# Kernel optimization log

Measured on AMD Instinct MI355X. Metric: run time of the kernel, lower is better.

The kernel has to match this reference:

```python
import jax, jax.numpy as jnp
import numpy as np

N = 50000      # nodes
E = 800000     # edges (avg degree 16)
H = 4          # attention heads
F_IN = 256     # input feature dim
D = 64         # per-head hidden/out dim (hidden*H = 256 chains into next layer)
NEG_SLOPE = 0.2  # DGL GATConv default leaky_relu slope


def setup_inputs() -> dict:
    key = jax.random.key(0)
    ks = jax.random.split(key, 12)
    inp = {
        "features": jax.random.normal(ks[0], (N, F_IN), jnp.float32),
        "src": jax.random.randint(ks[1], (E,), 0, N, jnp.int32),
        "dst": jax.random.randint(ks[2], (E,), 0, N, jnp.int32),
    }
    dims = [(F_IN, D), (H * D, D), (H * D, D)]
    for i, (fin, dout) in enumerate(dims):
        sc = 1.0 / np.sqrt(fin)
        inp[f"W{i+1}"] = jax.random.normal(ks[3 + 3 * i], (fin, H * dout), jnp.float32) * sc
        inp[f"al{i+1}"] = jax.random.normal(ks[4 + 3 * i], (H, dout), jnp.float32) * 0.1
        inp[f"ar{i+1}"] = jax.random.normal(ks[5 + 3 * i], (H, dout), jnp.float32) * 0.1
        inp[f"b{i+1}"] = jnp.zeros((H * dout,), jnp.float32)
    return inp


def gat_layer(h, src, dst, W, al, ar, b, act):
    n = h.shape[0]
    feat = (h @ W).reshape(n, H, -1)                     # [N, H, D]
    el = jnp.sum(feat * al, axis=-1)                     # [N, H]
    er = jnp.sum(feat * ar, axis=-1)                     # [N, H]
    e = jax.nn.leaky_relu(el[src] + er[dst], NEG_SLOPE)  # [E, H]
    # segment (per-dst) softmax over incoming edges
    m = jax.ops.segment_max(e, dst, num_segments=n)      # [N, H]
    ex = jnp.exp(e - m[dst])
    s = jax.ops.segment_sum(ex, dst, num_segments=n)
    alpha = ex / jnp.maximum(s[dst], 1e-9)               # [E, H]
    # weighted scatter-aggregate of source features
    out = jax.ops.segment_sum(feat[src] * alpha[..., None], dst, num_segments=n)  # [N, H, D]
    out = out + b.reshape(1, H, -1)
    if act:
        out = jax.nn.elu(out)
    return out.reshape(n, -1)                            # flatten(1): concat heads


def reference(features, src, dst, W1, al1, ar1, b1, W2, al2, ar2, b2, W3, al3, ar3, b3):
    h = gat_layer(features, src, dst, W1, al1, ar1, b1, act=True)
    h = gat_layer(h, src, dst, W2, al2, ar2, b2, act=True)
    h = gat_layer(h, src, dst, W3, al3, ar3, b3, act=False)
    return h  # [N, H*D] = [50000, 256]
```

## Files before the change

### kernel.cpp

```cpp
#include <hip/hip_runtime.h>
#include <hip/hip_bf16.h>
#include <cstdint>


#define FEAT 256
#define NHEAD 4

typedef short short8 __attribute__((ext_vector_type(8)));
typedef float f32x4 __attribute__((ext_vector_type(4)));

__device__ __forceinline__ ushort f2bf(float v) {
    uint u = __float_as_uint(v);
    uint r = (u + 0x7fffu + ((u >> 16) & 1u)) >> 16;
    return (ushort)r;
}
__device__ __forceinline__ float bf2f(ushort h) {
    return __uint_as_float(((uint)h) << 16);
}

__global__ void hist_kernel(const int* __restrict__ dst, int* __restrict__ deg, int E) {
    int e = blockIdx.x * 256 + threadIdx.x;
    if (e < E) atomicAdd(&deg[dst[e]], 1);
}

__global__ void scan_block(const int* __restrict__ deg, int* __restrict__ offs,
                           int* __restrict__ bsums, int n) {
    __shared__ int s[256];
    int i = blockIdx.x * 256 + threadIdx.x;
    int v = (i < n) ? deg[i] : 0;
    s[threadIdx.x] = v; __syncthreads();
    #pragma unroll
    for (int off = 1; off < 256; off <<= 1) {
        int t = (threadIdx.x >= off) ? s[threadIdx.x - off] : 0;
        __syncthreads();
        s[threadIdx.x] += t;
        __syncthreads();
    }
    if (i < n) offs[i] = s[threadIdx.x] - v;
    if (threadIdx.x == 255) bsums[blockIdx.x] = s[255];
}

__global__ void scan_sums(int* __restrict__ bsums, int nb) {
    __shared__ int s[256];
    int v = (threadIdx.x < nb) ? bsums[threadIdx.x] : 0;
    s[threadIdx.x] = v; __syncthreads();
    #pragma unroll
    for (int off = 1; off < 256; off <<= 1) {
        int t = (threadIdx.x >= off) ? s[threadIdx.x - off] : 0;
        __syncthreads();
        s[threadIdx.x] += t;
        __syncthreads();
    }
    if (threadIdx.x < nb) bsums[threadIdx.x] = s[threadIdx.x] - v;
}

__global__ void scan_add(int* __restrict__ offs, int* __restrict__ cursor,
                         const int* __restrict__ bsums, int n, int total) {
    int i = blockIdx.x * 256 + threadIdx.x;
    if (i < n) {
        int o = offs[i] + bsums[i >> 8];
        offs[i] = o;
        cursor[i] = o;
    }
    if (i == 0) offs[n] = total;
}

__global__ void scatter_kernel(const int* __restrict__ src, const int* __restrict__ dst,
                               int* __restrict__ cursor, int* __restrict__ csr_src, int E) {
    int e = blockIdx.x * 256 + threadIdx.x;
    if (e < E) {
        int d = dst[e];
        int pos = atomicAdd(&cursor[d], 1);
        csr_src[pos] = src[e];
    }
}

__global__ void wprep3_kernel(const float* __restrict__ W0, const float* __restrict__ W1,
                              const float* __restrict__ W2,
                              ushort* __restrict__ Wh0, ushort* __restrict__ Wl0,
                              ushort* __restrict__ Wh1, ushort* __restrict__ Wl1,
                              ushort* __restrict__ Wh2, ushort* __restrict__ Wl2) {
    const float* W = (blockIdx.y == 0) ? W0 : (blockIdx.y == 1) ? W1 : W2;
    ushort* Wh = (blockIdx.y == 0) ? Wh0 : (blockIdx.y == 1) ? Wh1 : Wh2;
    ushort* Wl = (blockIdx.y == 0) ? Wl0 : (blockIdx.y == 1) ? Wl1 : Wl2;
    int n = blockIdx.x;
    int k = threadIdx.x;
    float v = W[(size_t)k * FEAT + n];
    ushort h = f2bf(v);
    float r = v - bf2f(h);
    Wh[(size_t)n * FEAT + k] = h;
    Wl[(size_t)n * FEAT + k] = f2bf(r);
}

__global__ void fsplit_kernel(const float* __restrict__ A, ushort* __restrict__ Ah,
                              ushort* __restrict__ Al, int total8) {
    int i = blockIdx.x * 256 + threadIdx.x;
    if (i >= total8) return;
    const float4* p = (const float4*)(A + (size_t)i * 8);
    float4 a = p[0], b = p[1];
    float v[8] = {a.x, a.y, a.z, a.w, b.x, b.y, b.z, b.w};
    ushort hi[8], lo[8];
    #pragma unroll
    for (int t = 0; t < 8; ++t) {
        hi[t] = f2bf(v[t]);
        lo[t] = f2bf(v[t] - bf2f(hi[t]));
    }
    *(short8*)(Ah + (size_t)i * 8) = *(short8*)hi;
    *(short8*)(Al + (size_t)i * 8) = *(short8*)lo;
}

#define GBM 128
#define GBK 32
#define LDK 40
#define NKIT (FEAT / GBK)

__global__ __launch_bounds__(256) void gemm_fused(const ushort* __restrict__ Ahg,
                                                  const ushort* __restrict__ Alg,
                                                  const ushort* __restrict__ Whg,
                                                  const ushort* __restrict__ Wlg,
                                                  const float* __restrict__ alv,
                                                  const float* __restrict__ arv,
                                                  ushort* __restrict__ featB,
                                                  float* __restrict__ el,
                                                  float* __restrict__ er, int M) {
    __shared__ ushort Ah[2][GBM][LDK];
    __shared__ ushort Al[2][GBM][LDK];

    const int tid  = threadIdx.x;
    const int lane = tid & 63;
    const int wid  = tid >> 6;
    const int row0 = blockIdx.x * GBM;

    const int arow = tid >> 1;
    const int achk = (tid & 1) * 16;
    const bool aok = (row0 + arow) < M;
    const ushort* ApH = Ahg + (size_t)(row0 + arow) * FEAT + achk;
    const ushort* ApL = Alg + (size_t)(row0 + arow) * FEAT + achk;

    const int fr = lane & 15;
    const int fk = (lane >> 4) * 8;
    const int q  = lane >> 4;

    f32x4 acc[8][4];
    #pragma unroll
    for (int i = 0; i < 8; ++i)
        #pragma unroll
        for (int j = 0; j < 4; ++j) {
            f32x4 z = {0.f, 0.f, 0.f, 0.f};
            acc[i][j] = z;
        }

    const short8 z8 = {0, 0, 0, 0, 0, 0, 0, 0};

    {
        short8 h0 = aok ? *(const short8*)(ApH)     : z8;
        short8 h1 = aok ? *(const short8*)(ApH + 8) : z8;
        short8 l0 = aok ? *(const short8*)(ApL)     : z8;
        short8 l1 = aok ? *(const short8*)(ApL + 8) : z8;
        *(short8*)&Ah[0][arow][achk]     = h0;
        *(short8*)&Ah[0][arow][achk + 8] = h1;
        *(short8*)&Al[0][arow][achk]     = l0;
        *(short8*)&Al[0][arow][achk + 8] = l1;
    }

    #pragma unroll
    for (int t = 0; t < NKIT; ++t) {
        const int cur = t & 1;
        const int k0 = t * GBK;
        short8 h0 = z8, h1 = z8, l0 = z8, l1 = z8;
        if (t + 1 < NKIT && aok) {
            h0 = *(const short8*)(ApH + k0 + GBK);
            h1 = *(const short8*)(ApH + k0 + GBK + 8);
            l0 = *(const short8*)(ApL + k0 + GBK);
            l1 = *(const short8*)(ApL + k0 + GBK + 8);
        }
        short8 bfh[4], bfl[4];
        #pragma unroll
        for (int nt = 0; nt < 4; ++nt) {
            size_t boff = (size_t)(wid * 64 + nt * 16 + fr) * FEAT + k0 + fk;
            bfh[nt] = *(const short8*)(Whg + boff);
            bfl[nt] = *(const short8*)(Wlg + boff);
        }

        __syncthreads();

        #pragma unroll
        for (int mt = 0; mt < 8; ++mt) {
            short8 afh = *(const short8*)&Ah[cur][mt * 16 + fr][fk];
            short8 afl = *(const short8*)&Al[cur][mt * 16 + fr][fk];
            #pragma unroll
            for (int nt = 0; nt < 4; ++nt) {
                acc[mt][nt] = __builtin_amdgcn_mfma_f32_16x16x32_bf16(
                    afh, bfh[nt], acc[mt][nt], 0, 0, 0);
                acc[mt][nt] = __builtin_amdgcn_mfma_f32_16x16x32_bf16(
                    afh, bfl[nt], acc[mt][nt], 0, 0, 0);
                acc[mt][nt] = __builtin_amdgcn_mfma_f32_16x16x32_bf16(
                    afl, bfh[nt], acc[mt][nt], 0, 0, 0);
            }
        }
        if (t + 1 < NKIT) {
            *(short8*)&Ah[cur ^ 1][arow][achk]     = h0;
            *(short8*)&Ah[cur ^ 1][arow][achk + 8] = h1;
            *(short8*)&Al[cur ^ 1][arow][achk]     = l0;
            *(short8*)&Al[cur ^ 1][arow][achk + 8] = l1;
        }
    }

    float al4[4], ar4[4];
    #pragma unroll
    for (int nt = 0; nt < 4; ++nt) {
        al4[nt] = alv[wid * 64 + nt * 16 + fr];
        ar4[nt] = arv[wid * 64 + nt * 16 + fr];
    }
    #pragma unroll
    for (int mt = 0; mt < 8; ++mt) {
        #pragma unroll
        for (int r = 0; r < 4; ++r) {
            int row = row0 + mt * 16 + q * 4 + r;
            bool ok = row < M;
            float pl = 0.f, pr = 0.f;
            #pragma unroll
            for (int nt = 0; nt < 4; ++nt) {
                float v = acc[mt][nt][r];
                if (ok) featB[(size_t)row * FEAT + wid * 64 + nt * 16 + fr] = f2bf(v);
                pl = fmaf(v, al4[nt], pl);
                pr = fmaf(v, ar4[nt], pr);
            }
            #pragma unroll
            for (int o = 1; o < 16; o <<= 1) {
                pl += __shfl_xor(pl, o, 64);
                pr += __shfl_xor(pr, o, 64);
            }
            if (ok && fr == 0) {
                el[(size_t)row * NHEAD + wid] = pl;
                er[(size_t)row * NHEAD + wid] = pr;
            }
        }
    }
}

__global__ __launch_bounds__(256) void agg_kernel5(const ushort* __restrict__ featB,
                                                   const float* __restrict__ el,
                                                   const float* __restrict__ er,
                                                   const int* __restrict__ offs,
                                                   const int* __restrict__ csr_src,
                                                   const float* __restrict__ bias,
                                                   float* __restrict__ outF,
                                                   ushort* __restrict__ outH,
                                                   ushort* __restrict__ outL,
                                                   int act, int n) {
    int node = blockIdx.x * 4 + (threadIdx.x >> 6);
    if (node >= n) return;
    int lane = threadIdx.x & 63;
    int h   = lane >> 4;
    int j16 = lane & 15;
    int l31 = lane & 31;
    int par = lane >> 5;
    int fb  = l31 * 8;
    int hh  = l31 >> 3;
    int start = offs[node];
    int deg = offs[node + 1] - start;
    float erh = er[node * NHEAD + h];

    float m = -1e30f, ssum = 0.f;
    float a0 = 0.f, a1 = 0.f, a2 = 0.f, a3 = 0.f;
    float a4 = 0.f, a5 = 0.f, a6 = 0.f, a7 = 0.f;
    int sidx = (j16 < deg) ? csr_src[start + j16] : 0;

    for (int p0 = 0; p0 < deg; p0 += 16) {
        int pn = p0 + 16 + j16;
        int sidx_nx = (pn < deg) ? csr_src[start + pn] : 0;
        float e = -1e30f;
        if (p0 + j16 < deg) {
            float t = el[sidx * NHEAD + h] + erh;
            e = (t > 0.f) ? t : 0.2f * t;
        }
        float cm = e;
        #pragma unroll
        for (int o = 1; o < 16; o <<= 1) cm = fmaxf(cm, __shfl_xor(cm, o, 64));
        float newm = fmaxf(m, cm);
        float sc = __expf(m - newm);
        m = newm;
        ssum *= sc;
        float w = __expf(e - m);
        ssum += w;
        float scA = __shfl(sc, hh * 16, 64);
        a0 *= scA; a1 *= scA; a2 *= scA; a3 *= scA;
        a4 *= scA; a5 *= scA; a6 *= scA; a7 *= scA;
        int cnt = min(16, deg - p0);
        int iters = (cnt + 1) >> 1;
        for (int i = 0; i < iters; ++i) {
            int j0 = 2 * i + par;
            int sj = __shfl(sidx, j0, 16);
            float wj = __shfl(w, hh * 16 + j0, 64);
            short8 v = *(const short8*)(featB + (size_t)sj * FEAT + fb);
            a0 = fmaf(wj, bf2f((ushort)v[0]), a0);
            a1 = fmaf(wj, bf2f((ushort)v[1]), a1);
            a2 = fmaf(wj, bf2f((ushort)v[2]), a2);
            a3 = fmaf(wj, bf2f((ushort)v[3]), a3);
            a4 = fmaf(wj, bf2f((ushort)v[4]), a4);
            a5 = fmaf(wj, bf2f((ushort)v[5]), a5);
            a6 = fmaf(wj, bf2f((ushort)v[6]), a6);
            a7 = fmaf(wj, bf2f((ushort)v[7]), a7);
        }
        sidx = sidx_nx;
    }
    a0 += __shfl_xor(a0, 32, 64);
    a1 += __shfl_xor(a1, 32, 64);
    a2 += __shfl_xor(a2, 32, 64);
    a3 += __shfl_xor(a3, 32, 64);
    a4 += __shfl_xor(a4, 32, 64);
    a5 += __shfl_xor(a5, 32, 64);
    a6 += __shfl_xor(a6, 32, 64);
    a7 += __shfl_xor(a7, 32, 64);

    float st = ssum;
    #pragma unroll
    for (int o = 1; o < 16; o <<= 1) st += __shfl_xor(st, o, 64);
    float stA = __shfl(st, hh * 16, 64);
    if (par == 0) {
        float inv = 1.f / fmaxf(stA, 1e-9f);
        float4 b0 = *(const float4*)(bias + fb);
        float4 b1 = *(const float4*)(bias + fb + 4);
        float o0 = fmaf(a0, inv, b0.x);
        float o1 = fmaf(a1, inv, b0.y);
        float o2 = fmaf(a2, inv, b0.z);
        float o3 = fmaf(a3, inv, b0.w);
        float o4 = fmaf(a4, inv, b1.x);
        float o5 = fmaf(a5, inv, b1.y);
        float o6 = fmaf(a6, inv, b1.z);
        float o7 = fmaf(a7, inv, b1.w);
        if (act) {
            o0 = (o0 > 0.f) ? o0 : expm1f(o0);
            o1 = (o1 > 0.f) ? o1 : expm1f(o1);
            o2 = (o2 > 0.f) ? o2 : expm1f(o2);
            o3 = (o3 > 0.f) ? o3 : expm1f(o3);
            o4 = (o4 > 0.f) ? o4 : expm1f(o4);
            o5 = (o5 > 0.f) ? o5 : expm1f(o5);
            o6 = (o6 > 0.f) ? o6 : expm1f(o6);
            o7 = (o7 > 0.f) ? o7 : expm1f(o7);
        }
        if (outF) {
            *((float4*)(outF + (size_t)node * FEAT + fb))     = make_float4(o0, o1, o2, o3);
            *((float4*)(outF + (size_t)node * FEAT + fb + 4)) = make_float4(o4, o5, o6, o7);
        } else {
            ushort hi[8], lo[8];
            float ov[8] = {o0, o1, o2, o3, o4, o5, o6, o7};
            #pragma unroll
            for (int k = 0; k < 8; ++k) {
                hi[k] = f2bf(ov[k]);
                lo[k] = f2bf(ov[k] - bf2f(hi[k]));
            }
            *(short8*)(outH + (size_t)node * FEAT + fb) = *(short8*)hi;
            *(short8*)(outL + (size_t)node * FEAT + fb) = *(short8*)lo;
        }
    }
}

extern "C" void kernel_launch(void* const* d_in, const int* in_sizes, int n_in,
                              void* d_out, int out_size, void* d_ws, size_t ws_size,
                              hipStream_t stream) {
    const float* features = (const float*)d_in[0];
    const int*   src      = (const int*)d_in[1];
    const int*   dst      = (const int*)d_in[2];
    const int N = in_sizes[0] / FEAT;
    const int E = in_sizes[1];

    char* ws = (char*)d_ws;
    size_t off = 0;
    auto carve = [&](size_t bytes) -> void* {
        void* p = ws + off;
        off = (off + bytes + 255) & ~(size_t)255;
        return p;
    };
    int*    deg     = (int*)carve((size_t)N * 4);
    int*    offs    = (int*)carve((size_t)(N + 1) * 4);
    int*    cursor  = (int*)carve((size_t)N * 4);
    int*    bsums   = (int*)carve(4096);
    int*    csr_src = (int*)carve((size_t)E * 4);
    float*  el      = (float*)carve((size_t)N * NHEAD * 4);
    float*  er      = (float*)carve((size_t)N * NHEAD * 4);
    ushort* featB   = (ushort*)carve((size_t)N * FEAT * 2);
    ushort* inAh    = (ushort*)carve((size_t)N * FEAT * 2);
    ushort* inAl    = (ushort*)carve((size_t)N * FEAT * 2);
    ushort* Wh[3], *Wl[3];
    for (int i = 0; i < 3; ++i) {
        Wh[i] = (ushort*)carve((size_t)FEAT * FEAT * 2);
        Wl[i] = (ushort*)carve((size_t)FEAT * FEAT * 2);
    }

    const int nbE = (E + 255) / 256;
    const int nbN = (N + 255) / 256;

    hipMemsetAsync(deg, 0, (size_t)N * 4, stream);
    hist_kernel<<<nbE, 256, 0, stream>>>(dst, deg, E);
    scan_block<<<nbN, 256, 0, stream>>>(deg, offs, bsums, N);
    scan_sums<<<1, 256, 0, stream>>>(bsums, nbN);
    scan_add<<<nbN, 256, 0, stream>>>(offs, cursor, bsums, N, E);
    scatter_kernel<<<nbE, 256, 0, stream>>>(src, dst, cursor, csr_src, E);
    dim3 wgrid(FEAT, 3);
    wprep3_kernel<<<wgrid, FEAT, 0, stream>>>((const float*)d_in[3], (const float*)d_in[7],
                                              (const float*)d_in[11],
                                              Wh[0], Wl[0], Wh[1], Wl[1], Wh[2], Wl[2]);
    const int total8 = N * FEAT / 8;
    fsplit_kernel<<<(total8 + 255) / 256, 256, 0, stream>>>(features, inAh, inAl, total8);

    const int gemmBlocks = (N + GBM - 1) / GBM;
    const int nodeBlocks = (N + 3) / 4;

    gemm_fused<<<gemmBlocks, 256, 0, stream>>>(inAh, inAl, Wh[0], Wl[0],
                                               (const float*)d_in[4], (const float*)d_in[5],
                                               featB, el, er, N);
    agg_kernel5<<<nodeBlocks, 256, 0, stream>>>(featB, el, er, offs, csr_src,
                                                (const float*)d_in[6],
                                                (float*)nullptr, inAh, inAl, 1, N);
    gemm_fused<<<gemmBlocks, 256, 0, stream>>>(inAh, inAl, Wh[1], Wl[1],
                                               (const float*)d_in[8], (const float*)d_in[9],
                                               featB, el, er, N);
    agg_kernel5<<<nodeBlocks, 256, 0, stream>>>(featB, el, er, offs, csr_src,
                                                (const float*)d_in[10],
                                                (float*)nullptr, inAh, inAl, 1, N);
    gemm_fused<<<gemmBlocks, 256, 0, stream>>>(inAh, inAl, Wh[2], Wl[2],
                                               (const float*)d_in[12], (const float*)d_in[13],
                                               featB, el, er, N);
    agg_kernel5<<<nodeBlocks, 256, 0, stream>>>(featB, el, er, offs, csr_src,
                                                (const float*)d_in[14],
                                                (float*)d_out, (ushort*)nullptr, (ushort*)nullptr, 0, N);
}
```

Measured before the change: 474.0 us.

## Fuse fp32 hi/lo bf16 split into first-layer GEMM and halve GEMM row tile

```diff
diff --git a/kernel.cpp b/kernel.cpp
--- a/kernel.cpp
+++ b/kernel.cpp
@@ -92,24 +92,7 @@
     Wl[(size_t)n * FEAT + k] = f2bf(r);
 }
 
-__global__ void fsplit_kernel(const float* __restrict__ A, ushort* __restrict__ Ah,
-                              ushort* __restrict__ Al, int total8) {
-    int i = blockIdx.x * 256 + threadIdx.x;
-    if (i >= total8) return;
-    const float4* p = (const float4*)(A + (size_t)i * 8);
-    float4 a = p[0], b = p[1];
-    float v[8] = {a.x, a.y, a.z, a.w, b.x, b.y, b.z, b.w};
-    ushort hi[8], lo[8];
-    #pragma unroll
-    for (int t = 0; t < 8; ++t) {
-        hi[t] = f2bf(v[t]);
-        lo[t] = f2bf(v[t] - bf2f(hi[t]));
-    }
-    *(short8*)(Ah + (size_t)i * 8) = *(short8*)hi;
-    *(short8*)(Al + (size_t)i * 8) = *(short8*)lo;
-}
-
-#define GBM 128
+#define GBM 64
 #define GBK 32
 #define LDK 40
 #define NKIT (FEAT / GBK)
@@ -131,8 +114,8 @@
     const int wid  = tid >> 6;
     const int row0 = blockIdx.x * GBM;
 
-    const int arow = tid >> 1;
-    const int achk = (tid & 1) * 16;
+    const int arow = tid >> 2;
+    const int achk = (tid & 3) * 8;
     const bool aok = (row0 + arow) < M;
     const ushort* ApH = Ahg + (size_t)(row0 + arow) * FEAT + achk;
     const ushort* ApL = Alg + (size_t)(row0 + arow) * FEAT + achk;
@@ -141,9 +124,9 @@
     const int fk = (lane >> 4) * 8;
     const int q  = lane >> 4;
 
-    f32x4 acc[8][4];
-    #pragma unroll
-    for (int i = 0; i < 8; ++i)
+    f32x4 acc[4][4];
+    #pragma unroll
+    for (int i = 0; i < 4; ++i)
         #pragma unroll
         for (int j = 0; j < 4; ++j) {
             f32x4 z = {0.f, 0.f, 0.f, 0.f};
@@ -153,26 +136,20 @@
     const short8 z8 = {0, 0, 0, 0, 0, 0, 0, 0};
 
     {
-        short8 h0 = aok ? *(const short8*)(ApH)     : z8;
-        short8 h1 = aok ? *(const short8*)(ApH + 8) : z8;
-        short8 l0 = aok ? *(const short8*)(ApL)     : z8;
-        short8 l1 = aok ? *(const short8*)(ApL + 8) : z8;
-        *(short8*)&Ah[0][arow][achk]     = h0;
-        *(short8*)&Ah[0][arow][achk + 8] = h1;
-        *(short8*)&Al[0][arow][achk]     = l0;
-        *(short8*)&Al[0][arow][achk + 8] = l1;
+        short8 a_h = aok ? *(const short8*)(ApH) : z8;
+        short8 a_l = aok ? *(const short8*)(ApL) : z8;
+        *(short8*)&Ah[0][arow][achk] = a_h;
+        *(short8*)&Al[0][arow][achk] = a_l;
     }
 
     #pragma unroll
     for (int t = 0; t < NKIT; ++t) {
         const int cur = t & 1;
         const int k0 = t * GBK;
-        short8 h0 = z8, h1 = z8, l0 = z8, l1 = z8;
+        short8 a_h = z8, a_l = z8;
         if (t + 1 < NKIT && aok) {
-            h0 = *(const short8*)(ApH + k0 + GBK);
-            h1 = *(const short8*)(ApH + k0 + GBK + 8);
-            l0 = *(const short8*)(ApL + k0 + GBK);
-            l1 = *(const short8*)(ApL + k0 + GBK + 8);
+            a_h = *(const short8*)(ApH + k0 + GBK);
+            a_l = *(const short8*)(ApL + k0 + GBK);
         }
         short8 bfh[4], bfl[4];
         #pragma unroll
@@ -185,7 +162,7 @@
         __syncthreads();
 
         #pragma unroll
-        for (int mt = 0; mt < 8; ++mt) {
+        for (int mt = 0; mt < 4; ++mt) {
             short8 afh = *(const short8*)&Ah[cur][mt * 16 + fr][fk];
             short8 afl = *(const short8*)&Al[cur][mt * 16 + fr][fk];
             #pragma unroll
@@ -199,10 +176,8 @@
             }
         }
         if (t + 1 < NKIT) {
-            *(short8*)&Ah[cur ^ 1][arow][achk]     = h0;
-            *(short8*)&Ah[cur ^ 1][arow][achk + 8] = h1;
-            *(short8*)&Al[cur ^ 1][arow][achk]     = l0;
-            *(short8*)&Al[cur ^ 1][arow][achk + 8] = l1;
+            *(short8*)&Ah[cur ^ 1][arow][achk] = a_h;
+            *(short8*)&Al[cur ^ 1][arow][achk] = a_l;
         }
     }
 
@@ -213,7 +188,130 @@
         ar4[nt] = arv[wid * 64 + nt * 16 + fr];
     }
     #pragma unroll
-    for (int mt = 0; mt < 8; ++mt) {
+    for (int mt = 0; mt < 4; ++mt) {
+        #pragma unroll
+        for (int r = 0; r < 4; ++r) {
+            int row = row0 + mt * 16 + q * 4 + r;
+            bool ok = row < M;
+            float pl = 0.f, pr = 0.f;
+            #pragma unroll
+            for (int nt = 0; nt < 4; ++nt) {
+                float v = acc[mt][nt][r];
+                if (ok) featB[(size_t)row * FEAT + wid * 64 + nt * 16 + fr] = f2bf(v);
+                pl = fmaf(v, al4[nt], pl);
+                pr = fmaf(v, ar4[nt], pr);
+            }
+            #pragma unroll
+            for (int o = 1; o < 16; o <<= 1) {
+                pl += __shfl_xor(pl, o, 64);
+                pr += __shfl_xor(pr, o, 64);
+            }
+            if (ok && fr == 0) {
+                el[(size_t)row * NHEAD + wid] = pl;
+                er[(size_t)row * NHEAD + wid] = pr;
+            }
+        }
+    }
+}
+
+__global__ __launch_bounds__(256) void gemm_fused_f32a(const float* __restrict__ Af,
+                                                       const ushort* __restrict__ Whg,
+                                                       const ushort* __restrict__ Wlg,
+                                                       const float* __restrict__ alv,
+                                                       const float* __restrict__ arv,
+                                                       ushort* __restrict__ featB,
+                                                       float* __restrict__ el,
+                                                       float* __restrict__ er, int M) {
+    __shared__ ushort Ah[2][GBM][LDK];
+    __shared__ ushort Al[2][GBM][LDK];
+
+    const int tid  = threadIdx.x;
+    const int lane = tid & 63;
+    const int wid  = tid >> 6;
+    const int row0 = blockIdx.x * GBM;
+
+    const int arow = tid >> 2;
+    const int achk = (tid & 3) * 8;
+    const bool aok = (row0 + arow) < M;
+    const float* Ap = Af + (size_t)(row0 + arow) * FEAT + achk;
+
+    const int fr = lane & 15;
+    const int fk = (lane >> 4) * 8;
+    const int q  = lane >> 4;
+
+    f32x4 acc[4][4];
+    #pragma unroll
+    for (int i = 0; i < 4; ++i)
+        #pragma unroll
+        for (int j = 0; j < 4; ++j) {
+            f32x4 z = {0.f, 0.f, 0.f, 0.f};
+            acc[i][j] = z;
+        }
+
+    const float4 z4 = make_float4(0.f, 0.f, 0.f, 0.f);
+
+    auto split_store = [&](int buf, float4 f0, float4 f1) {
+        float v[8] = {f0.x, f0.y, f0.z, f0.w, f1.x, f1.y, f1.z, f1.w};
+        ushort hi[8], lo[8];
+        #pragma unroll
+        for (int k = 0; k < 8; ++k) {
+            hi[k] = f2bf(v[k]);
+            lo[k] = f2bf(v[k] - bf2f(hi[k]));
+        }
+        *(short8*)&Ah[buf][arow][achk] = *(short8*)hi;
+        *(short8*)&Al[buf][arow][achk] = *(short8*)lo;
+    };
+
+    {
+        float4 f0 = aok ? *(const float4*)(Ap)     : z4;
+        float4 f1 = aok ? *(const float4*)(Ap + 4) : z4;
+        split_store(0, f0, f1);
+    }
+
+    #pragma unroll
+    for (int t = 0; t < NKIT; ++t) {
+        const int cur = t & 1;
+        const int k0 = t * GBK;
+        float4 f0 = z4, f1 = z4;
+        if (t + 1 < NKIT && aok) {
+            f0 = *(const float4*)(Ap + k0 + GBK);
+            f1 = *(const float4*)(Ap + k0 + GBK + 4);
+        }
+        short8 bfh[4], bfl[4];
+        #pragma unroll
+        for (int nt = 0; nt < 4; ++nt) {
+            size_t boff = (size_t)(wid * 64 + nt * 16 + fr) * FEAT + k0 + fk;
+            bfh[nt] = *(const short8*)(Whg + boff);
+            bfl[nt] = *(const short8*)(Wlg + boff);
+        }
+
+        __syncthreads();
+
+        #pragma unroll
+        for (int mt = 0; mt < 4; ++mt) {
+            short8 afh = *(const short8*)&Ah[cur][mt * 16 + fr][fk];
+            short8 afl = *(const short8*)&Al[cur][mt * 16 + fr][fk];
+            #pragma unroll
+            for (int nt = 0; nt < 4; ++nt) {
+                acc[mt][nt] = __builtin_amdgcn_mfma_f32_16x16x32_bf16(
+                    afh, bfh[nt], acc[mt][nt], 0, 0, 0);
+                acc[mt][nt] = __builtin_amdgcn_mfma_f32_16x16x32_bf16(
+                    afh, bfl[nt], acc[mt][nt], 0, 0, 0);
+                acc[mt][nt] = __builtin_amdgcn_mfma_f32_16x16x32_bf16(
+                    afl, bfh[nt], acc[mt][nt], 0, 0, 0);
+            }
+        }
+        if (t + 1 < NKIT) split_store(cur ^ 1, f0, f1);
+    }
+
+    float al4[4], ar4[4];
+    #pragma unroll
+    for (int nt = 0; nt < 4; ++nt) {
+        al4[nt] = alv[wid * 64 + nt * 16 + fr];
+        ar4[nt] = arv[wid * 64 + nt * 16 + fr];
+    }
+    #pragma unroll
+    for (int mt = 0; mt < 4; ++mt) {
         #pragma unroll
         for (int r = 0; r < 4; ++r) {
             int row = row0 + mt * 16 + q * 4 + r;
@@ -402,15 +500,13 @@
     wprep3_kernel<<<wgrid, FEAT, 0, stream>>>((const float*)d_in[3], (const float*)d_in[7],
                                               (const float*)d_in[11],
                                               Wh[0], Wl[0], Wh[1], Wl[1], Wh[2], Wl[2]);
-    const int total8 = N * FEAT / 8;
-    fsplit_kernel<<<(total8 + 255) / 256, 256, 0, stream>>>(features, inAh, inAl, total8);
 
     const int gemmBlocks = (N + GBM - 1) / GBM;
     const int nodeBlocks = (N + 3) / 4;
 
-    gemm_fused<<<gemmBlocks, 256, 0, stream>>>(inAh, inAl, Wh[0], Wl[0],
-                                               (const float*)d_in[4], (const float*)d_in[5],
-                                               featB, el, er, N);
+    gemm_fused_f32a<<<gemmBlocks, 256, 0, stream>>>(features, Wh[0], Wl[0],
+                                                    (const float*)d_in[4], (const float*)d_in[5],
+                                                    featB, el, er, N);
     agg_kernel5<<<nodeBlocks, 256, 0, stream>>>(featB, el, er, offs, csr_src,
                                                 (const float*)d_in[6],
                                                 (float*)nullptr, inAh, inAl, 1, N);
```

After: 444.9 us. -6.1%, faster.
